# Performance work log

Hardware: AMD Instinct MI355X
Metric: run time of the kernel (lower is better)

Reference implementation:

```python
import jax, jax.numpy as jnp
import numpy as np

K_NEIGHBOURS = 40  # includes self; self is dropped after top-k


def setup_inputs() -> dict:
    key = jax.random.key(0)
    ks = jax.random.split(key, 4)
    B, V, F_in = 4, 4096, 64
    P, S, F_out = 64, 4, 64
    x = jax.random.normal(ks[0], (B, V, F_in), dtype=jnp.float32)
    Wf = jax.random.normal(ks[1], (F_in, P), dtype=jnp.float32) / np.sqrt(F_in)
    bf = jnp.zeros((P,), dtype=jnp.float32)
    Ws = jax.random.normal(ks[2], (F_in, S), dtype=jnp.float32) / np.sqrt(F_in)
    bs = jnp.zeros((S,), dtype=jnp.float32)
    Wo = jax.random.normal(ks[3], (F_in + 2 * P, F_out), dtype=jnp.float32) / np.sqrt(F_in + 2 * P)
    bo = jnpp = jnp.zeros((F_out,), dtype=jnp.float32)
    return {"x": x, "Wf": Wf, "bf": bf, "Ws": Ws, "bs": bs, "Wo": Wo, "bo": bo}


def _euclidean_squared(c):
    # c: [B, V, S] -> [B, V, V] squared pairwise distances
    sq = jnp.sum(c * c, axis=-1)  # [B, V]
    d2 = sq[:, :, None] + sq[:, None, :] - 2.0 * jnp.einsum('bvs,bus->bvu', c, c)
    return d2


def reference(x, Wf, bf, Ws, bs, Wo, bo):
    # learned spatial coordinates and propagated features
    coords = x @ Ws + bs            # [B, V, S]
    feats = x @ Wf + bf             # [B, V, P]

    d2 = _euclidean_squared(coords)                 # [B, V, V]
    neg_vals, idx = jax.lax.top_k(-d2, K_NEIGHBOURS)  # closest first (self at 0)
    nbr_idx = idx[:, :, 1:]                         # [B, V, K-1]
    dist = -neg_vals[:, :, 1:]                      # [B, V, K-1] (>= 0)

    # gauss_of_lin(d * 10) = exp(-|10 d|)
    w = jnp.exp(-jnp.abs(dist * 10.0))              # [B, V, K-1]

    # gather neighbour features per batch: [B, V, K-1, P]
    nf = jax.vmap(lambda f, i: f[i])(feats, nbr_idx)
    nf = nf * w[..., None]

    collected = jnp.concatenate([jnp.max(nf, axis=2), jnp.mean(nf, axis=2)], axis=-1)  # [B, V, 2P]
    updated = jnp.concatenate([x, collected], axis=-1)  # [B, V, F_in + 2P]
    return jnp.tanh(updated @ Wo + bo)
```

## Files before the change

### kernel.cpp

```cpp
#include <hip/hip_runtime.h>
#include <cmath>

#define BB  4
#define VV  4096
#define KK  40
#define FIN 64

typedef float v2f __attribute__((ext_vector_type(2)));

__global__ __launch_bounds__(256) void prep_kernel(
    const float* __restrict__ x, const float* __restrict__ Wf,
    const float* __restrict__ bf, const float* __restrict__ Ws,
    const float* __restrict__ bs,
    float* __restrict__ coords, float* __restrict__ sq,
    float* __restrict__ feats)
{
    int lane = threadIdx.x & 63;
    int wid  = threadIdx.x >> 6;
    int row0 = (blockIdx.x * 4 + wid) * 4;
    const float* xr = x + (size_t)row0 * FIN;

    float rx0 = xr[lane];
    float rx1 = xr[64  + lane];
    float rx2 = xr[128 + lane];
    float rx3 = xr[192 + lane];

    float a0 = 0.f, a1 = 0.f, a2 = 0.f, a3 = 0.f;
    #pragma unroll
    for (int k = 0; k < FIN; ++k) {
        float wf = Wf[k * 64 + lane];
        a0 = fmaf(__uint_as_float(
             __builtin_amdgcn_readlane(__float_as_uint(rx0), k)), wf, a0);
        a1 = fmaf(__uint_as_float(
             __builtin_amdgcn_readlane(__float_as_uint(rx1), k)), wf, a1);
        a2 = fmaf(__uint_as_float(
             __builtin_amdgcn_readlane(__float_as_uint(rx2), k)), wf, a2);
        a3 = fmaf(__uint_as_float(
             __builtin_amdgcn_readlane(__float_as_uint(rx3), k)), wf, a3);
    }
    float bfl = bf[lane];
    feats[(size_t)(row0 + 0) * 64 + lane] = a0 + bfl;
    feats[(size_t)(row0 + 1) * 64 + lane] = a1 + bfl;
    feats[(size_t)(row0 + 2) * 64 + lane] = a2 + bfl;
    feats[(size_t)(row0 + 3) * 64 + lane] = a3 + bfl;

    int r  = lane >> 4;
    int s  = (lane >> 2) & 3;
    int kc = lane & 3;
    const float* xrr = x + (size_t)(row0 + r) * FIN + kc * 16;
    const float* wsr = Ws + kc * 16 * 4 + s;
    float c = 0.f;
    #pragma unroll
    for (int k = 0; k < 16; ++k)
        c = fmaf(xrr[k], wsr[k * 4], c);
    c += __shfl_xor(c, 1, 64);
    c += __shfl_xor(c, 2, 64);
    float val = c + bs[s];
    if ((lane & 3) == 0) coords[(size_t)(row0 + r) * 4 + s] = val;
    float p = val * val;
    p += __shfl_xor(p, 4, 64);
    p += __shfl_xor(p, 8, 64);
    if ((lane & 15) == 0) sq[row0 + r] = p;
}

__device__ __forceinline__ unsigned umed3(unsigned a, unsigned b, unsigned c)
{
    unsigned d;
    asm("v_med3_u32 %0, %1, %2, %3" : "=v"(d) : "v"(a), "v"(b), "v"(c));
    return d;
}

__device__ __forceinline__ unsigned bfi_key(unsigned maskv, unsigned d2b,
                                            unsigned u)
{
    unsigned d;
    asm("v_bfi_b32 %0, %1, %2, %3" : "=v"(d) : "v"(maskv), "v"(d2b), "v"(u));
    return d;
}

__device__ __forceinline__ int cnt_lt4(unsigned m0, unsigned m1,
                                       unsigned m2, unsigned m3,
                                       unsigned cand)
{
    return (int)__popcll(__ballot(m0 < cand))
         + (int)__popcll(__ballot(m1 < cand))
         + (int)__popcll(__ballot(m2 < cand))
         + (int)__popcll(__ballot(m3 < cand));
}

__device__ __forceinline__ unsigned select_thresh(unsigned m0, unsigned m1,
                                                  unsigned m2, unsigned m3)
{
    unsigned M = 0u;
    #pragma unroll
    for (int bit = 30; bit >= 12; --bit) {
        unsigned cand = M | (1u << bit);
        if (cnt_lt4(m0, m1, m2, m3, cand) <= 39) M = cand;
    }
    unsigned Msel = M | 0xFFFu;
    if (cnt_lt4(m0, m1, m2, m3, M + 4096u) != 40) {
        #pragma unroll
        for (int bit = 11; bit >= 0; --bit) {
            unsigned cand = M | (1u << bit);
            if (cnt_lt4(m0, m1, m2, m3, cand) <= 39) M = cand;
        }
        Msel = M;
    }
    return Msel;
}

__device__ __forceinline__ void compact4(unsigned m0, unsigned m1,
                                         unsigned m2, unsigned m3,
                                         unsigned Msel, uint2* dst)
{
    unsigned mn = m0;
    #pragma unroll
    for (int off = 32; off >= 1; off >>= 1) {
        unsigned o = __shfl_xor(mn, off, 64);
        mn = o < mn ? o : mn;
    }
    int base = 0;
    unsigned kk = m0;
    #pragma unroll
    for (int i = 0; i < 4; ++i) {
        bool pred = (kk <= Msel) && (kk != mn);
        unsigned long long mask = __ballot(pred);
        unsigned pos = (unsigned)base +
            __builtin_amdgcn_mbcnt_hi((unsigned)(mask >> 32),
                __builtin_amdgcn_mbcnt_lo((unsigned)mask, 0u));
        if (pred) {
            float d2a = __uint_as_float(kk & 0xFFFFF000u);
            float w   = __expf(-10.f * d2a);
            dst[pos] = make_uint2((kk & 4095u) << 8, __float_as_uint(w));
        }
        base += (int)__popcll(mask);
        kk = (i == 0) ? m1 : (i == 1) ? m2 : m3;
    }
}

__global__ __launch_bounds__(256, 4) void gravnet_kernel(
    const float* __restrict__ x, const float* __restrict__ coords,
    const float* __restrict__ sq, const float* __restrict__ feats,
    const float* __restrict__ Wo, const float* __restrict__ bo,
    float* __restrict__ out)
{
    int lane = threadIdx.x & 63;
    int w    = threadIdx.x >> 6;
    int bid  = (int)((blockIdx.x & 7) * 128 + (blockIdx.x >> 3));
    int gw   = bid * 4 + w;
    int qb   = gw * 4;
    int b    = qb >> 12;
    int v0   = qb & (VV - 1);

    __shared__ __align__(16) char smem[12288];
    uint2* s_nb  = (uint2*)(smem + w * 3072);
    float* s_upd = (float*)(smem + w * 3072);

    const float4* cb  = (const float4*)(coords + (size_t)b * VV * 4);
    const float*  sqb = sq + (size_t)b * VV;

    float4 cq0 = cb[v0],     cq1 = cb[v0 + 1];
    float4 cq2 = cb[v0 + 2], cq3 = cb[v0 + 3];
    v2f nxA = (v2f){-2.f * cq0.x, -2.f * cq1.x};
    v2f nyA = (v2f){-2.f * cq0.y, -2.f * cq1.y};
    v2f nzA = (v2f){-2.f * cq0.z, -2.f * cq1.z};
    v2f nwA = (v2f){-2.f * cq0.w, -2.f * cq1.w};
    v2f hsA = (v2f){sqb[v0], sqb[v0 + 1]};
    v2f nxB = (v2f){-2.f * cq2.x, -2.f * cq3.x};
    v2f nyB = (v2f){-2.f * cq2.y, -2.f * cq3.y};
    v2f nzB = (v2f){-2.f * cq2.z, -2.f * cq3.z};
    v2f nwB = (v2f){-2.f * cq2.w, -2.f * cq3.w};
    v2f hsB = (v2f){sqb[v0 + 2], sqb[v0 + 3]};

    unsigned k00 = ~0u, k01 = ~0u, k02 = ~0u, k03 = ~0u;
    unsigned k10 = ~0u, k11 = ~0u, k12 = ~0u, k13 = ~0u;
    unsigned k20 = ~0u, k21 = ~0u, k22 = ~0u, k23 = ~0u;
    unsigned k30 = ~0u, k31 = ~0u, k32 = ~0u, k33 = ~0u;

    unsigned maskv = 0xFFFFF000u;

    #pragma unroll 4
    for (int i = 0; i < 64; ++i) {
        int u = i * 64 + lane;
        float4 cu = cb[u];
        float squ = sqb[u];
        v2f accA = hsA + (v2f){squ, squ};
        accA = __builtin_elementwise_fma(nxA, (v2f){cu.x, cu.x}, accA);
        accA = __builtin_elementwise_fma(nyA, (v2f){cu.y, cu.y}, accA);
        accA = __builtin_elementwise_fma(nzA, (v2f){cu.z, cu.z}, accA);
        accA = __builtin_elementwise_fma(nwA, (v2f){cu.w, cu.w}, accA);
        v2f accB = hsB + (v2f){squ, squ};
        accB = __builtin_elementwise_fma(nxB, (v2f){cu.x, cu.x}, accB);
        accB = __builtin_elementwise_fma(nyB, (v2f){cu.y, cu.y}, accB);
        accB = __builtin_elementwise_fma(nzB, (v2f){cu.z, cu.z}, accB);
        accB = __builtin_elementwise_fma(nwB, (v2f){cu.w, cu.w}, accB);

        {
            float d2 = fmaxf(accA.x, 0.f);
            unsigned k = bfi_key(maskv, __float_as_uint(d2), (unsigned)u);
            unsigned n1 = umed3(k00, k01, k);
            unsigned n2 = umed3(k01, k02, k);
            unsigned n3 = umed3(k02, k03, k);
            k00 = min(k00, k); k01 = n1; k02 = n2; k03 = n3;
        }
        {
            float d2 = fmaxf(accA.y, 0.f);
            unsigned k = bfi_key(maskv, __float_as_uint(d2), (unsigned)u);
            unsigned n1 = umed3(k10, k11, k);
            unsigned n2 = umed3(k11, k12, k);
            unsigned n3 = umed3(k12, k13, k);
            k10 = min(k10, k); k11 = n1; k12 = n2; k13 = n3;
        }
        {
            float d2 = fmaxf(accB.x, 0.f);
            unsigned k = bfi_key(maskv, __float_as_uint(d2), (unsigned)u);
            unsigned n1 = umed3(k20, k21, k);
            unsigned n2 = umed3(k21, k22, k);
            unsigned n3 = umed3(k22, k23, k);
            k20 = min(k20, k); k21 = n1; k22 = n2; k23 = n3;
        }
        {
            float d2 = fmaxf(accB.y, 0.f);
            unsigned k = bfi_key(maskv, __float_as_uint(d2), (unsigned)u);
            unsigned n1 = umed3(k30, k31, k);
            unsigned n2 = umed3(k31, k32, k);
            unsigned n3 = umed3(k32, k33, k);
            k30 = min(k30, k); k31 = n1; k32 = n2; k33 = n3;
        }
    }

    compact4(k00, k01, k02, k03,
             select_thresh(k00, k01, k02, k03), &s_nb[0 * KK]);
    compact4(k10, k11, k12, k13,
             select_thresh(k10, k11, k12, k13), &s_nb[1 * KK]);
    compact4(k20, k21, k22, k23,
             select_thresh(k20, k21, k22, k23), &s_nb[2 * KK]);
    compact4(k30, k31, k32, k33,
             select_thresh(k30, k31, k32, k33), &s_nb[3 * KK]);

    const float* fb  = feats + (size_t)b * VV * 64;
    const char*  fbl = (const char*)(fb + lane);
    const uint4* nb0 = (const uint4*)&s_nb[0 * KK];
    const uint4* nb1 = (const uint4*)&s_nb[1 * KK];
    const uint4* nb2 = (const uint4*)&s_nb[2 * KK];
    const uint4* nb3 = (const uint4*)&s_nb[3 * KK];
    v2f vmax01 = (v2f){-INFINITY, -INFINITY};
    v2f vsum01 = (v2f){0.f, 0.f};
    v2f vmax23 = (v2f){-INFINITY, -INFINITY};
    v2f vsum23 = (v2f){0.f, 0.f};
    #pragma unroll 2
    for (int jp = 0; jp < 19; ++jp) {
        uint4 a = nb0[jp];
        uint4 c = nb1[jp];
        uint4 e = nb2[jp];
        uint4 g = nb3[jp];
        float f0a = *(const float*)(fbl + a.x);
        float f1a = *(const float*)(fbl + c.x);
        float f2a = *(const float*)(fbl + e.x);
        float f3a = *(const float*)(fbl + g.x);
        float f0b = *(const float*)(fbl + a.z);
        float f1b = *(const float*)(fbl + c.z);
        float f2b = *(const float*)(fbl + e.z);
        float f3b = *(const float*)(fbl + g.z);
        v2f ga01 = (v2f){f0a, f1a} *
                   (v2f){__uint_as_float(a.y), __uint_as_float(c.y)};
        v2f gb01 = (v2f){f0b, f1b} *
                   (v2f){__uint_as_float(a.w), __uint_as_float(c.w)};
        v2f ga23 = (v2f){f2a, f3a} *
                   (v2f){__uint_as_float(e.y), __uint_as_float(g.y)};
        v2f gb23 = (v2f){f2b, f3b} *
                   (v2f){__uint_as_float(e.w), __uint_as_float(g.w)};
        vmax01 = __builtin_elementwise_max(vmax01,
                 __builtin_elementwise_max(ga01, gb01));
        vsum01 += ga01 + gb01;
        vmax23 = __builtin_elementwise_max(vmax23,
                 __builtin_elementwise_max(ga23, gb23));
        vsum23 += ga23 + gb23;
    }
    {
        uint2 n0 = s_nb[0 * KK + 38];
        uint2 n1 = s_nb[1 * KK + 38];
        uint2 n2 = s_nb[2 * KK + 38];
        uint2 n3 = s_nb[3 * KK + 38];
        float f0 = *(const float*)(fbl + n0.x);
        float f1 = *(const float*)(fbl + n1.x);
        float f2 = *(const float*)(fbl + n2.x);
        float f3 = *(const float*)(fbl + n3.x);
        v2f g01 = (v2f){f0, f1} *
                  (v2f){__uint_as_float(n0.y), __uint_as_float(n1.y)};
        v2f g23 = (v2f){f2, f3} *
                  (v2f){__uint_as_float(n2.y), __uint_as_float(n3.y)};
        vmax01 = __builtin_elementwise_max(vmax01, g01);
        vsum01 += g01;
        vmax23 = __builtin_elementwise_max(vmax23, g23);
        vsum23 += g23;
    }

    int q0g = qb, q1g = qb + 1, q2g = qb + 2, q3g = qb + 3;
    float* sb = s_upd;
    *(float4*)&sb[lane * 4] =
        make_float4(x[(size_t)q0g * 64 + lane], x[(size_t)q1g * 64 + lane],
                    x[(size_t)q2g * 64 + lane], x[(size_t)q3g * 64 + lane]);
    *(float4*)&sb[256 + lane * 4] =
        make_float4(vmax01.x, vmax01.y, vmax23.x, vmax23.y);
    *(float4*)&sb[512 + lane * 4] =
        make_float4(vsum01.x * (1.0f / 39.0f), vsum01.y * (1.0f / 39.0f),
                    vsum23.x * (1.0f / 39.0f), vsum23.y * (1.0f / 39.0f));

    float bol = bo[lane];
    v2f acc01 = (v2f){bol, bol};
    v2f acc23 = (v2f){bol, bol};
    #pragma unroll 8
    for (int j = 0; j < 192; ++j) {
        float wo = Wo[j * 64 + lane];
        float4 up = *(const float4*)&sb[j * 4];
        acc01 = __builtin_elementwise_fma((v2f){up.x, up.y},
                                          (v2f){wo, wo}, acc01);
        acc23 = __builtin_elementwise_fma((v2f){up.z, up.w},
                                          (v2f){wo, wo}, acc23);
    }
    float e0t = __expf(2.f * acc01.x);
    float e1t = __expf(2.f * acc01.y);
    float e2t = __expf(2.f * acc23.x);
    float e3t = __expf(2.f * acc23.y);
    out[(size_t)q0g * 64 + lane] = 1.f - __fdividef(2.f, e0t + 1.f);
    out[(size_t)q1g * 64 + lane] = 1.f - __fdividef(2.f, e1t + 1.f);
    out[(size_t)q2g * 64 + lane] = 1.f - __fdividef(2.f, e2t + 1.f);
    out[(size_t)q3g * 64 + lane] = 1.f - __fdividef(2.f, e3t + 1.f);
}

extern "C" void kernel_launch(void* const* d_in, const int* in_sizes, int n_in,
                              void* d_out, int out_size, void* d_ws, size_t ws_size,
                              hipStream_t stream)
{
    (void)in_sizes; (void)n_in; (void)out_size; (void)ws_size;
    const float* x  = (const float*)d_in[0];
    const float* Wf = (const float*)d_in[1];
    const float* bf = (const float*)d_in[2];
    const float* Ws = (const float*)d_in[3];
    const float* bs = (const float*)d_in[4];
    const float* Wo = (const float*)d_in[5];
    const float* bo = (const float*)d_in[6];
    float* out = (float*)d_out;

    float* coords = (float*)d_ws;
    float* sq     = coords + (size_t)BB * VV * 4;
    float* feats  = sq + (size_t)BB * VV;

    prep_kernel<<<BB * VV / 16, 256, 0, stream>>>(x, Wf, bf, Ws, bs,
                                                  coords, sq, feats);
    gravnet_kernel<<<BB * VV / 16, 256, 0, stream>>>(x, coords, sq, feats,
                                                     Wo, bo, out);
}
```

Baseline: 118.8 us.

## Interleave threshold selection across four queries and halve prep rows per wave

The prep kernel now handles two rows per wave instead of four and launches twice as many blocks, with an occupancy hint in its launch bounds. In the main kernel, the four per-query bit-search threshold selections run interleaved, so their ballots and popcounts can overlap. The four min-reductions are also hoisted and interleaved. The gather loop uses 32-bit offset arithmetic and is unrolled by four instead of two. These changes target latency from serial dependent ballot chains and launch underutilisation, at the cost of higher register pressure.

```diff
diff --git a/kernel.cpp b/kernel.cpp
--- a/kernel.cpp
+++ b/kernel.cpp
@@ -8,7 +8,7 @@
 
 typedef float v2f __attribute__((ext_vector_type(2)));
 
-__global__ __launch_bounds__(256) void prep_kernel(
+__global__ __launch_bounds__(256, 8) void prep_kernel(
     const float* __restrict__ x, const float* __restrict__ Wf,
     const float* __restrict__ bf, const float* __restrict__ Ws,
     const float* __restrict__ bs,
@@ -17,15 +17,13 @@
 {
     int lane = threadIdx.x & 63;
     int wid  = threadIdx.x >> 6;
-    int row0 = (blockIdx.x * 4 + wid) * 4;
+    int row0 = (blockIdx.x * 4 + wid) * 2;
     const float* xr = x + (size_t)row0 * FIN;
 
     float rx0 = xr[lane];
-    float rx1 = xr[64  + lane];
-    float rx2 = xr[128 + lane];
-    float rx3 = xr[192 + lane];
-
-    float a0 = 0.f, a1 = 0.f, a2 = 0.f, a3 = 0.f;
+    float rx1 = xr[64 + lane];
+
+    float a0 = 0.f, a1 = 0.f;
     #pragma unroll
     for (int k = 0; k < FIN; ++k) {
         float wf = Wf[k * 64 + lane];
@@ -33,34 +31,29 @@
              __builtin_amdgcn_readlane(__float_as_uint(rx0), k)), wf, a0);
         a1 = fmaf(__uint_as_float(
              __builtin_amdgcn_readlane(__float_as_uint(rx1), k)), wf, a1);
-        a2 = fmaf(__uint_as_float(
-             __builtin_amdgcn_readlane(__float_as_uint(rx2), k)), wf, a2);
-        a3 = fmaf(__uint_as_float(
-             __builtin_amdgcn_readlane(__float_as_uint(rx3), k)), wf, a3);
     }
     float bfl = bf[lane];
     feats[(size_t)(row0 + 0) * 64 + lane] = a0 + bfl;
     feats[(size_t)(row0 + 1) * 64 + lane] = a1 + bfl;
-    feats[(size_t)(row0 + 2) * 64 + lane] = a2 + bfl;
-    feats[(size_t)(row0 + 3) * 64 + lane] = a3 + bfl;
-
-    int r  = lane >> 4;
-    int s  = (lane >> 2) & 3;
-    int kc = lane & 3;
-    const float* xrr = x + (size_t)(row0 + r) * FIN + kc * 16;
-    const float* wsr = Ws + kc * 16 * 4 + s;
+
+    int r  = lane >> 5;
+    int s  = (lane >> 3) & 3;
+    int kc = lane & 7;
+    const float* xrr = x + (size_t)(row0 + r) * FIN + kc * 8;
+    const float* wsr = Ws + kc * 8 * 4 + s;
     float c = 0.f;
     #pragma unroll
-    for (int k = 0; k < 16; ++k)
+    for (int k = 0; k < 8; ++k)
         c = fmaf(xrr[k], wsr[k * 4], c);
     c += __shfl_xor(c, 1, 64);
     c += __shfl_xor(c, 2, 64);
+    c += __shfl_xor(c, 4, 64);
     float val = c + bs[s];
-    if ((lane & 3) == 0) coords[(size_t)(row0 + r) * 4 + s] = val;
+    if ((lane & 7) == 0) coords[(size_t)(row0 + r) * 4 + s] = val;
     float p = val * val;
-    p += __shfl_xor(p, 4, 64);
     p += __shfl_xor(p, 8, 64);
-    if ((lane & 15) == 0) sq[row0 + r] = p;
+    p += __shfl_xor(p, 16, 64);
+    if ((lane & 31) == 0) sq[row0 + r] = p;
 }
 
 __device__ __forceinline__ unsigned umed3(unsigned a, unsigned b, unsigned c)
@@ -88,37 +81,68 @@
          + (int)__popcll(__ballot(m3 < cand));
 }
 
-__device__ __forceinline__ unsigned select_thresh(unsigned m0, unsigned m1,
-                                                  unsigned m2, unsigned m3)
-{
-    unsigned M = 0u;
+__device__ __forceinline__ void select_thresh4(
+    unsigned m00, unsigned m01, unsigned m02, unsigned m03,
+    unsigned m10, unsigned m11, unsigned m12, unsigned m13,
+    unsigned m20, unsigned m21, unsigned m22, unsigned m23,
+    unsigned m30, unsigned m31, unsigned m32, unsigned m33,
+    unsigned& Ms0, unsigned& Ms1, unsigned& Ms2, unsigned& Ms3)
+{
+    unsigned M0 = 0u, M1 = 0u, M2 = 0u, M3 = 0u;
     #pragma unroll
     for (int bit = 30; bit >= 12; --bit) {
-        unsigned cand = M | (1u << bit);
-        if (cnt_lt4(m0, m1, m2, m3, cand) <= 39) M = cand;
-    }
-    unsigned Msel = M | 0xFFFu;
-    if (cnt_lt4(m0, m1, m2, m3, M + 4096u) != 40) {
+        unsigned b = 1u << bit;
+        unsigned c0 = M0 | b, c1 = M1 | b, c2 = M2 | b, c3 = M3 | b;
+        int n0 = cnt_lt4(m00, m01, m02, m03, c0);
+        int n1 = cnt_lt4(m10, m11, m12, m13, c1);
+        int n2 = cnt_lt4(m20, m21, m22, m23, c2);
+        int n3 = cnt_lt4(m30, m31, m32, m33, c3);
+        if (n0 <= 39) M0 = c0;
+        if (n1 <= 39) M1 = c1;
+        if (n2 <= 39) M2 = c2;
+        if (n3 <= 39) M3 = c3;
+    }
+    Ms0 = M0 | 0xFFFu; Ms1 = M1 | 0xFFFu;
+    Ms2 = M2 | 0xFFFu; Ms3 = M3 | 0xFFFu;
+    if (cnt_lt4(m00, m01, m02, m03, M0 + 4096u) != 40) {
         #pragma unroll
         for (int bit = 11; bit >= 0; --bit) {
-            unsigned cand = M | (1u << bit);
-            if (cnt_lt4(m0, m1, m2, m3, cand) <= 39) M = cand;
-        }
-        Msel = M;
-    }
-    return Msel;
+            unsigned cand = M0 | (1u << bit);
+            if (cnt_lt4(m00, m01, m02, m03, cand) <= 39) M0 = cand;
+        }
+        Ms0 = M0;
+    }
+    if (cnt_lt4(m10, m11, m12, m13, M1 + 4096u) != 40) {
+        #pragma unroll
+        for (int bit = 11; bit >= 0; --bit) {
+            unsigned cand = M1 | (1u << bit);
+            if (cnt_lt4(m10, m11, m12, m13, cand) <= 39) M1 = cand;
+        }
+        Ms1 = M1;
+    }
+    if (cnt_lt4(m20, m21, m22, m23, M2 + 4096u) != 40) {
+        #pragma unroll
+        for (int bit = 11; bit >= 0; --bit) {
+            unsigned cand = M2 | (1u << bit);
+            if (cnt_lt4(m20, m21, m22, m23, cand) <= 39) M2 = cand;
+        }
+        Ms2 = M2;
+    }
+    if (cnt_lt4(m30, m31, m32, m33, M3 + 4096u) != 40) {
+        #pragma unroll
+        for (int bit = 11; bit >= 0; --bit) {
+            unsigned cand = M3 | (1u << bit);
+            if (cnt_lt4(m30, m31, m32, m33, cand) <= 39) M3 = cand;
+        }
+        Ms3 = M3;
+    }
 }
 
 __device__ __forceinline__ void compact4(unsigned m0, unsigned m1,
                                          unsigned m2, unsigned m3,
-                                         unsigned Msel, uint2* dst)
-{
-    unsigned mn = m0;
-    #pragma unroll
-    for (int off = 32; off >= 1; off >>= 1) {
-        unsigned o = __shfl_xor(mn, off, 64);
-        mn = o < mn ? o : mn;
-    }
+                                         unsigned Msel, unsigned mn,
+                                         uint2* dst)
+{
     int base = 0;
     unsigned kk = m0;
     #pragma unroll
@@ -229,17 +253,28 @@
         }
     }
 
-    compact4(k00, k01, k02, k03,
-             select_thresh(k00, k01, k02, k03), &s_nb[0 * KK]);
-    compact4(k10, k11, k12, k13,
-             select_thresh(k10, k11, k12, k13), &s_nb[1 * KK]);
-    compact4(k20, k21, k22, k23,
-             select_thresh(k20, k21, k22, k23), &s_nb[2 * KK]);
-    compact4(k30, k31, k32, k33,
-             select_thresh(k30, k31, k32, k33), &s_nb[3 * KK]);
+    unsigned mn0 = k00, mn1 = k10, mn2 = k20, mn3 = k30;
+    #pragma unroll
+    for (int off = 32; off >= 1; off >>= 1) {
+        unsigned o0 = __shfl_xor(mn0, off, 64);
+        unsigned o1 = __shfl_xor(mn1, off, 64);
+        unsigned o2 = __shfl_xor(mn2, off, 64);
+        unsigned o3 = __shfl_xor(mn3, off, 64);
+        mn0 = min(mn0, o0); mn1 = min(mn1, o1);
+        mn2 = min(mn2, o2); mn3 = min(mn3, o3);
+    }
+
+    unsigned Ms0, Ms1, Ms2, Ms3;
+    select_thresh4(k00, k01, k02, k03, k10, k11, k12, k13,
+                   k20, k21, k22, k23, k30, k31, k32, k33,
+                   Ms0, Ms1, Ms2, Ms3);
+    compact4(k00, k01, k02, k03, Ms0, mn0, &s_nb[0 * KK]);
+    compact4(k10, k11, k12, k13, Ms1, mn1, &s_nb[1 * KK]);
+    compact4(k20, k21, k22, k23, Ms2, mn2, &s_nb[2 * KK]);
+    compact4(k30, k31, k32, k33, Ms3, mn3, &s_nb[3 * KK]);
 
     const float* fb  = feats + (size_t)b * VV * 64;
-    const char*  fbl = (const char*)(fb + lane);
+    unsigned lane4 = (unsigned)lane << 2;
     const uint4* nb0 = (const uint4*)&s_nb[0 * KK];
     const uint4* nb1 = (const uint4*)&s_nb[1 * KK];
     const uint4* nb2 = (const uint4*)&s_nb[2 * KK];
@@ -248,20 +283,20 @@
     v2f vsum01 = (v2f){0.f, 0.f};
     v2f vmax23 = (v2f){-INFINITY, -INFINITY};
     v2f vsum23 = (v2f){0.f, 0.f};
-    #pragma unroll 2
+    #pragma unroll 4
     for (int jp = 0; jp < 19; ++jp) {
         uint4 a = nb0[jp];
         uint4 c = nb1[jp];
         uint4 e = nb2[jp];
         uint4 g = nb3[jp];
-        float f0a = *(const float*)(fbl + a.x);
-        float f1a = *(const float*)(fbl + c.x);
-        float f2a = *(const float*)(fbl + e.x);
-        float f3a = *(const float*)(fbl + g.x);
-        float f0b = *(const float*)(fbl + a.z);
-        float f1b = *(const float*)(fbl + c.z);
-        float f2b = *(const float*)(fbl + e.z);
-        float f3b = *(const float*)(fbl + g.z);
+        float f0a = *(const float*)((const char*)fb + (a.x + lane4));
+        float f1a = *(const float*)((const char*)fb + (c.x + lane4));
+        float f2a = *(const float*)((const char*)fb + (e.x + lane4));
+        float f3a = *(const float*)((const char*)fb + (g.x + lane4));
+        float f0b = *(const float*)((const char*)fb + (a.z + lane4));
+        float f1b = *(const float*)((const char*)fb + (c.z + lane4));
+        float f2b = *(const float*)((const char*)fb + (e.z + lane4));
+        float f3b = *(const float*)((const char*)fb + (g.z + lane4));
         v2f ga01 = (v2f){f0a, f1a} *
                    (v2f){__uint_as_float(a.y), __uint_as_float(c.y)};
         v2f gb01 = (v2f){f0b, f1b} *
@@ -282,10 +317,10 @@
         uint2 n1 = s_nb[1 * KK + 38];
         uint2 n2 = s_nb[2 * KK + 38];
         uint2 n3 = s_nb[3 * KK + 38];
-        float f0 = *(const float*)(fbl + n0.x);
-        float f1 = *(const float*)(fbl + n1.x);
-        float f2 = *(const float*)(fbl + n2.x);
-        float f3 = *(const float*)(fbl + n3.x);
+        float f0 = *(const float*)((const char*)fb + (n0.x + lane4));
+        float f1 = *(const float*)((const char*)fb + (n1.x + lane4));
+        float f2 = *(const float*)((const char*)fb + (n2.x + lane4));
+        float f3 = *(const float*)((const char*)fb + (n3.x + lane4));
         v2f g01 = (v2f){f0, f1} *
                   (v2f){__uint_as_float(n0.y), __uint_as_float(n1.y)};
         v2f g23 = (v2f){f2, f3} *
@@ -347,8 +382,8 @@
     float* sq     = coords + (size_t)BB * VV * 4;
     float* feats  = sq + (size_t)BB * VV;
 
-    prep_kernel<<<BB * VV / 16, 256, 0, stream>>>(x, Wf, bf, Ws, bs,
-                                                  coords, sq, feats);
+    prep_kernel<<<BB * VV / 8, 256, 0, stream>>>(x, Wf, bf, Ws, bs,
+                                                 coords, sq, feats);
     gravnet_kernel<<<BB * VV / 16, 256, 0, stream>>>(x, coords, sq, feats,
                                                      Wo, bo, out);
 }
```

Result: no change. 119.1 us, median of 2 (+0.2%).
